# Kernel optimization log

Measured on AMD Instinct MI355X. Metric: run time of the kernel, lower is better.

Reference implementation:

```python
import jax, jax.numpy as jnp
import numpy as np

N, E = 20000, 320000
ATOM_IN, BOND_IN, HIDDEN, LAYERS = 64, 16, 256, 5
BN_EPS = 1e-5


def setup_inputs() -> dict:
    key = jax.random.key(0)
    ks = jax.random.split(key, 16)
    s = 0.05
    return {
        "x": jax.random.normal(ks[0], (N, ATOM_IN), jnp.float32),
        "edge_attr": jax.random.normal(ks[1], (E, BOND_IN), jnp.float32),
        "edge_index": jax.random.randint(ks[2], (2, E), 0, N, jnp.int32),
        "Wa": jax.random.normal(ks[3], (ATOM_IN, HIDDEN), jnp.float32) * s,
        "ba": jnp.zeros((HIDDEN,), jnp.float32),
        "We": jax.random.normal(ks[4], (BOND_IN, HIDDEN), jnp.float32) * s,
        "be": jnp.zeros((HIDDEN,), jnp.float32),
        "eps": jnp.zeros((LAYERS,), jnp.float32),  # train_eps=True, init 0
        "W1": jax.random.normal(ks[5], (LAYERS, HIDDEN, HIDDEN), jnp.float32) * s,
        "b1": jnp.zeros((LAYERS, HIDDEN), jnp.float32),
        "W2": jax.random.normal(ks[6], (LAYERS, HIDDEN, HIDDEN), jnp.float32) * s,
        "b2": jnp.zeros((LAYERS, HIDDEN), jnp.float32),
        "gamma": jnp.ones((LAYERS, HIDDEN), jnp.float32),
        "beta": jnp.zeros((LAYERS, HIDDEN), jnp.float32),
    }


def reference(x, edge_attr, edge_index, Wa, ba, We, be, eps, W1, b1, W2, b2, gamma, beta):
    src, dst = edge_index[0], edge_index[1]  # messages flow src -> dst (PyG x_j = x[src])
    h = x @ Wa + ba                          # [N, H] atom_proj
    e = edge_attr @ We + be                  # [E, H] edge_proj
    for l in range(LAYERS):
        # GINEConv: aggr = sum_j relu(x_j + e_ij); out = mlp((1+eps)*x_i + aggr)
        msg = jax.nn.relu(h[src] + e)                              # [E, H]
        aggr = jax.ops.segment_sum(msg, dst, num_segments=N)        # [N, H]
        z = (1.0 + eps[l]) * h + aggr
        z = jax.nn.relu(z @ W1[l] + b1[l]) @ W2[l] + b2[l]          # 2-layer MLP
        # BatchNorm1d over the node dimension (batch statistics)
        mu = jnp.mean(z, axis=0)
        var = jnp.var(z, axis=0)
        z = (z - mu) * jax.lax.rsqrt(var + BN_EPS) * gamma[l] + beta[l]
        z = jax.nn.relu(z)
        # dropout is identity in deterministic reference (eval)
        h = h + z  # residual
    return h
```

## Files before the change

kernel.cpp:

```cpp
#include <hip/hip_runtime.h>

typedef unsigned short u16;
typedef __attribute__((ext_vector_type(4))) float f32x4;
typedef __attribute__((ext_vector_type(8))) short s16x8;
typedef __attribute__((ext_vector_type(8))) unsigned short u16x8;
typedef __attribute__((ext_vector_type(4))) unsigned short u16x4;

__device__ inline float bf2f(u16 u) {
    unsigned v = ((unsigned)u) << 16;
    return __builtin_bit_cast(float, v);
}
__device__ inline u16 f2bf(float f) {
    unsigned u = __builtin_bit_cast(unsigned, f);
    unsigned r = (u + 0x7FFFu + ((u >> 16) & 1u)) >> 16;
    return (u16)r;
}

__global__ void count_kernel(const int* __restrict__ dst, int E, int* __restrict__ counts) {
    int e = blockIdx.x * 256 + threadIdx.x;
    if (e < E) atomicAdd(&counts[dst[e]], 1);
}

__global__ __launch_bounds__(1024) void scan_kernel(const int* __restrict__ counts,
    int* __restrict__ row_start, int* __restrict__ cursor, int NN) {
    __shared__ int sh[1024];
    const int tid = threadIdx.x;
    const int CH = (NN + 1023) / 1024;
    const int base = tid * CH;
    int sum = 0;
    for (int i = 0; i < CH; ++i) { int idx = base + i; if (idx < NN) sum += counts[idx]; }
    sh[tid] = sum; __syncthreads();
    for (int off = 1; off < 1024; off <<= 1) {
        int v = (tid >= off) ? sh[tid - off] : 0;
        __syncthreads();
        sh[tid] += v;
        __syncthreads();
    }
    int run = sh[tid] - sum;
    for (int i = 0; i < CH; ++i) {
        int idx = base + i;
        if (idx <= NN) {
            row_start[idx] = run;
            if (idx < NN) { cursor[idx] = run; run += counts[idx]; }
        }
    }
}

__global__ void pos_kernel(const int* __restrict__ src, const int* __restrict__ dst, int E,
    int* __restrict__ cursor, int* __restrict__ pos, int* __restrict__ src_perm) {
    int e = blockIdx.x * 256 + threadIdx.x;
    if (e < E) {
        int p = atomicAdd(&cursor[dst[e]], 1);
        pos[e] = p;
        src_perm[p] = src[e];
    }
}

__global__ void prep_kernel(const float* __restrict__ x, const float* __restrict__ Wa,
    const float* __restrict__ We, const float* __restrict__ be,
    const float* __restrict__ W1, const float* __restrict__ W2,
    u16* __restrict__ x_bf, u16* __restrict__ Wat, u16* __restrict__ Wet,
    u16* __restrict__ W1t, u16* __restrict__ W2t, int NN) {
    int i = blockIdx.x * 256 + threadIdx.x;
    const int S0 = NN * 16;
    if (i < S0) {
        f32x4 v = *(const f32x4*)(x + (size_t)i * 4);
        u16x4 o; o.x = f2bf(v[0]); o.y = f2bf(v[1]); o.z = f2bf(v[2]); o.w = f2bf(v[3]);
        *(u16x4*)(x_bf + (size_t)i * 4) = o;
        return;
    }
    i -= S0;
    if (i < 16384) { int n = i >> 6, k = i & 63; Wat[i] = f2bf(Wa[k * 256 + n]); return; }
    i -= 16384;
    if (i < 8192) {
        int n = i >> 5, k = i & 31;
        float v = (k < 16) ? We[k * 256 + n] : ((k == 16) ? be[n] : 0.f);
        Wet[i] = f2bf(v); return;
    }
    i -= 8192;
    if (i < 327680) { int l = i >> 16, r = i & 65535, n = r >> 8, k = r & 255;
        W1t[i] = f2bf(W1[(size_t)l * 65536 + k * 256 + n]); return; }
    i -= 327680;
    if (i < 327680) { int l = i >> 16, r = i & 65535, n = r >> 8, k = r & 255;
        W2t[i] = f2bf(W2[(size_t)l * 65536 + k * 256 + n]); return; }
}

__global__ void permute_pad_eattr_kernel(const float* __restrict__ ea, const int* __restrict__ pos,
                                         int E, u16* __restrict__ out) {
    int e = blockIdx.x * 256 + threadIdx.x;
    if (e >= E) return;
    const float* r = ea + (size_t)e * 16;
    f32x4 q0 = *(const f32x4*)(r + 0);
    f32x4 q1 = *(const f32x4*)(r + 4);
    f32x4 q2 = *(const f32x4*)(r + 8);
    f32x4 q3 = *(const f32x4*)(r + 12);
    u16x8 v0, v1, m, z;
#pragma unroll
    for (int j = 0; j < 4; ++j) {
        v0[j] = f2bf(q0[j]); v0[4 + j] = f2bf(q1[j]);
        v1[j] = f2bf(q2[j]); v1[4 + j] = f2bf(q3[j]);
        m[j] = 0; m[4 + j] = 0; z[j] = 0; z[4 + j] = 0;
    }
    m[0] = 0x3F80;
    u16* o = out + (size_t)pos[e] * 32;
    *(u16x8*)(o + 0) = v0;
    *(u16x8*)(o + 8) = v1;
    *(u16x8*)(o + 16) = m;
    *(u16x8*)(o + 24) = z;
}

__global__ __launch_bounds__(256) void gemm_h0_kernel(
    const u16* __restrict__ A, int lda, int M,
    const u16* __restrict__ Bt, int K,
    const float* __restrict__ bias,
    float* __restrict__ outF, u16* __restrict__ outB, int ldo) {
    __shared__ u16 As[128 * 32];
    __shared__ u16 Bs[128 * 32];
    const int tid = threadIdx.x, lane = tid & 63, wave = tid >> 6;
    const int m0 = blockIdx.x * 128, n0 = blockIdx.y * 128;
    const int wr = (wave >> 1) * 64, wc = (wave & 1) * 64;

    const f32x4 zero4 = {0.f, 0.f, 0.f, 0.f};
    f32x4 acc[4][4];
#pragma unroll
    for (int m = 0; m < 4; ++m)
#pragma unroll
        for (int n = 0; n < 4; ++n) acc[m][n] = zero4;

    for (int k0 = 0; k0 < K; k0 += 32) {
#pragma unroll
        for (int i = 0; i < 2; ++i) {
            int seg = i * 256 + tid;
            int row = seg >> 2, sk = seg & 3;
            int gr = m0 + row; gr = gr < M ? gr : M - 1;
            u16x8 va = *(const u16x8*)(A + (size_t)gr * lda + k0 + sk * 8);
            *(u16x8*)(&As[row * 32 + sk * 8]) = va;
            u16x8 vb = *(const u16x8*)(Bt + (size_t)(n0 + row) * K + k0 + sk * 8);
            *(u16x8*)(&Bs[row * 32 + sk * 8]) = vb;
        }
        __syncthreads();
        const int rsel = lane & 15, koff = (lane >> 4) * 8;
        s16x8 af[4], bf[4];
#pragma unroll
        for (int m = 0; m < 4; ++m) af[m] = *(const s16x8*)(&As[(wr + m * 16 + rsel) * 32 + koff]);
#pragma unroll
        for (int n = 0; n < 4; ++n) bf[n] = *(const s16x8*)(&Bs[(wc + n * 16 + rsel) * 32 + koff]);
#pragma unroll
        for (int m = 0; m < 4; ++m)
#pragma unroll
            for (int n = 0; n < 4; ++n)
                acc[m][n] = __builtin_amdgcn_mfma_f32_16x16x32_bf16(af[m], bf[n], acc[m][n], 0, 0, 0);
        __syncthreads();
    }

    const int cl = lane & 15, rq = lane >> 4;
#pragma unroll
    for (int n = 0; n < 4; ++n) {
        const int gcol = n0 + wc + n * 16 + cl;
        const float bv = bias[gcol];
#pragma unroll
        for (int m = 0; m < 4; ++m) {
#pragma unroll
            for (int j = 0; j < 4; ++j) {
                int grow = m0 + wr + m * 16 + rq * 4 + j;
                if (grow < M) {
                    float v = acc[m][n][j] + bv;
                    outF[(size_t)grow * ldo + gcol] = v;
                    outB[(size_t)grow * ldo + gcol] = f2bf(v);
                }
            }
        }
    }
}

__global__ __launch_bounds__(256) void mlp_fused_kernel(
    const u16* __restrict__ z, int M,
    const u16* __restrict__ W1t, const float* __restrict__ b1,
    const u16* __restrict__ W2t, const float* __restrict__ b2,
    u16* __restrict__ y2,
    float* __restrict__ colsum, float* __restrict__ colsumsq) {
    __shared__ u16 As[64 * 32];
    __shared__ u16 Bs[256 * 32];
    __shared__ u16 Ys[64 * 260];
    const int tid = threadIdx.x, lane = tid & 63, wave = tid >> 6;
    const int m0 = blockIdx.x * 64;
    const int wc = wave * 64;
    const int rsel = lane & 15, koff = (lane >> 4) * 8;
    const int cl = lane & 15, rq = lane >> 4;

    const f32x4 zero4 = {0.f, 0.f, 0.f, 0.f};
    f32x4 acc[4][4];
#pragma unroll
    for (int m = 0; m < 4; ++m)
#pragma unroll
        for (int n = 0; n < 4; ++n) acc[m][n] = zero4;

    for (int k0 = 0; k0 < 256; k0 += 32) {
        {
            int row = tid >> 2, sk = tid & 3;
            int gr = m0 + row; gr = gr < M ? gr : M - 1;
            u16x8 va = *(const u16x8*)(z + (size_t)gr * 256 + k0 + sk * 8);
            *(u16x8*)(&As[row * 32 + sk * 8]) = va;
        }
#pragma unroll
        for (int i = 0; i < 4; ++i) {
            int seg = i * 256 + tid;
            int row = seg >> 2, sk = seg & 3;
            u16x8 vb = *(const u16x8*)(W1t + (size_t)row * 256 + k0 + sk * 8);
            *(u16x8*)(&Bs[row * 32 + sk * 8]) = vb;
        }
        __syncthreads();
        s16x8 af[4], bf[4];
#pragma unroll
        for (int m = 0; m < 4; ++m) af[m] = *(const s16x8*)(&As[(m * 16 + rsel) * 32 + koff]);
#pragma unroll
        for (int n = 0; n < 4; ++n) bf[n] = *(const s16x8*)(&Bs[(wc + n * 16 + rsel) * 32 + koff]);
#pragma unroll
        for (int m = 0; m < 4; ++m)
#pragma unroll
            for (int n = 0; n < 4; ++n)
                acc[m][n] = __builtin_amdgcn_mfma_f32_16x16x32_bf16(af[m], bf[n], acc[m][n], 0, 0, 0);
        __syncthreads();
    }
#pragma unroll
    for (int n = 0; n < 4; ++n) {
        const int gcol = wc + n * 16 + cl;
        const float bv = b1[gcol];
#pragma unroll
        for (int m = 0; m < 4; ++m) {
#pragma unroll
            for (int j = 0; j < 4; ++j) {
                int row = m * 16 + rq * 4 + j;
                float v = fmaxf(acc[m][n][j] + bv, 0.f);
                Ys[row * 260 + gcol] = f2bf(v);
            }
        }
        acc[0][n] = zero4; acc[1][n] = zero4; acc[2][n] = zero4; acc[3][n] = zero4;
    }

    for (int k0 = 0; k0 < 256; k0 += 32) {
#pragma unroll
        for (int i = 0; i < 4; ++i) {
            int seg = i * 256 + tid;
            int row = seg >> 2, sk = seg & 3;
            u16x8 vb = *(const u16x8*)(W2t + (size_t)row * 256 + k0 + sk * 8);
            *(u16x8*)(&Bs[row * 32 + sk * 8]) = vb;
        }
        __syncthreads();
        s16x8 af[4], bf[4];
#pragma unroll
        for (int m = 0; m < 4; ++m) af[m] = *(const s16x8*)(&Ys[(m * 16 + rsel) * 260 + k0 + koff]);
#pragma unroll
        for (int n = 0; n < 4; ++n) bf[n] = *(const s16x8*)(&Bs[(wc + n * 16 + rsel) * 32 + koff]);
#pragma unroll
        for (int m = 0; m < 4; ++m)
#pragma unroll
            for (int n = 0; n < 4; ++n)
                acc[m][n] = __builtin_amdgcn_mfma_f32_16x16x32_bf16(af[m], bf[n], acc[m][n], 0, 0, 0);
        __syncthreads();
    }
#pragma unroll
    for (int n = 0; n < 4; ++n) {
        const int gcol = wc + n * 16 + cl;
        const float bv = b2[gcol];
        float s = 0.f, ss = 0.f;
#pragma unroll
        for (int m = 0; m < 4; ++m) {
#pragma unroll
            for (int j = 0; j < 4; ++j) {
                int row = m * 16 + rq * 4 + j;
                float v = acc[m][n][j] + bv;
                Ys[row * 260 + gcol] = f2bf(v);
                if (m0 + row < M) { s += v; ss += v * v; }
            }
        }
        s += __shfl_down(s, 32); ss += __shfl_down(ss, 32);
        s += __shfl_down(s, 16); ss += __shfl_down(ss, 16);
        if (rq == 0) {
            atomicAdd(&colsum[gcol], s);
            atomicAdd(&colsumsq[gcol], ss);
        }
    }
    __syncthreads();
    for (int r0 = 0; r0 < 64; r0 += 8) {
        int row = r0 + (tid >> 5);
        int gr = m0 + row;
        int cc = (tid & 31) * 8;
        if (gr < M) *(u16x8*)(y2 + (size_t)gr * 256 + cc) = *(u16x8*)(&Ys[row * 260 + cc]);
    }
}

__global__ __launch_bounds__(256) void agg_rc_kernel(
    const int* __restrict__ row_start, const int* __restrict__ src_perm,
    const u16* __restrict__ eap, const u16* __restrict__ Wet,
    const u16* __restrict__ h_bf, const float* __restrict__ h,
    const float* __restrict__ eps, int layer,
    u16* __restrict__ z_bf, int NN) {
    __shared__ u16 ET[4 * 16 * 264];
    const int tid = threadIdx.x;
    const int lane = tid & 63;
    const int wv = tid >> 6;
    const int rsel = lane & 15;
    const int q = lane >> 4;
    const int half = lane >> 5;
    const int c0 = (lane & 31) * 8;
    u16* et = &ET[wv * 16 * 264];

    s16x8 wf[16];
#pragma unroll
    for (int b = 0; b < 16; ++b)
        wf[b] = *(const s16x8*)(Wet + (b * 16 + rsel) * 32 + q * 8);

    const int node = blockIdx.x * 4 + wv;
    if (node >= NN) return;
    const int s0 = row_start[node], s1 = row_start[node + 1];

    const f32x4 zero4 = {0.f, 0.f, 0.f, 0.f};
    float a[8] = {0.f, 0.f, 0.f, 0.f, 0.f, 0.f, 0.f, 0.f};

    for (int e0 = s0; e0 < s1; e0 += 16) {
        const int ec = (e0 + rsel < s1) ? (e0 + rsel) : (s1 - 1);
        s16x8 eaf = *(const s16x8*)(eap + (size_t)ec * 32 + q * 8);
#pragma unroll
        for (int b = 0; b < 16; ++b) {
            f32x4 d = __builtin_amdgcn_mfma_f32_16x16x32_bf16(wf[b], eaf, zero4, 0, 0, 0);
            u16x4 w;
#pragma unroll
            for (int j = 0; j < 4; ++j) w[j] = f2bf(d[j]);
            *(u16x4*)(et + rsel * 264 + b * 16 + q * 4) = w;
        }
        const int cnt = (s1 - e0 < 16) ? (s1 - e0) : 16;
        for (int kk = 0; kk < cnt; kk += 4) {
            const int ka = kk + half, kb = kk + 2 + half;
            const bool v0 = ka < cnt, v1 = kb < cnt;
            const int ia = v0 ? (e0 + ka) : (s1 - 1);
            const int ib = v1 ? (e0 + kb) : (s1 - 1);
            const int sa = src_perm[ia];
            const int sb = src_perm[ib];
            u16x8 h0 = *(const u16x8*)(h_bf + (size_t)sa * 256 + c0);
            u16x8 h1 = *(const u16x8*)(h_bf + (size_t)sb * 256 + c0);
            u16x8 e8a = *(const u16x8*)(et + (v0 ? ka : 0) * 264 + c0);
            u16x8 e8b = *(const u16x8*)(et + (v1 ? kb : 0) * 264 + c0);
            const float m0 = v0 ? 1.f : 0.f;
            const float m1 = v1 ? 1.f : 0.f;
#pragma unroll
            for (int j = 0; j < 8; ++j) {
                a[j] += m0 * fmaxf(bf2f((u16)e8a[j]) + bf2f((u16)h0[j]), 0.f);
                a[j] += m1 * fmaxf(bf2f((u16)e8b[j]) + bf2f((u16)h1[j]), 0.f);
            }
        }
    }
#pragma unroll
    for (int j = 0; j < 8; ++j) a[j] += __shfl_xor(a[j], 32);
    if (half == 0) {
        const float c = 1.f + eps[layer];
        const f32x4 hr0 = *(const f32x4*)(h + (size_t)node * 256 + c0);
        const f32x4 hr1 = *(const f32x4*)(h + (size_t)node * 256 + c0 + 4);
        u16x8 z;
#pragma unroll
        for (int j = 0; j < 4; ++j) {
            z[j] = f2bf(c * hr0[j] + a[j]);
            z[4 + j] = f2bf(c * hr1[j] + a[4 + j]);
        }
        *(u16x8*)(z_bf + (size_t)node * 256 + c0) = z;
    }
}

__global__ __launch_bounds__(256) void bn_res_kernel(
    const u16* __restrict__ y2, const float* __restrict__ colsum,
    const float* __restrict__ colsumsq, const float* __restrict__ gamma,
    const float* __restrict__ beta, const float* __restrict__ hin,
    float* __restrict__ hout, u16* __restrict__ h_bf, int write_bf,
    float invN, int total4) {
    const int i = blockIdx.x * 256 + threadIdx.x;
    if (i >= total4) return;
    const size_t base = (size_t)i * 4;
    const int c0 = (int)(base & 255);
    u16x4 yv = *(const u16x4*)(y2 + base);
    f32x4 hv = *(const f32x4*)(hin + base);
    u16 ys[4] = {yv.x, yv.y, yv.z, yv.w};
    f32x4 res;
#pragma unroll
    for (int j = 0; j < 4; ++j) {
        const int c = c0 + j;
        const float mu = colsum[c] * invN;
        const float var = colsumsq[c] * invN - mu * mu;
        const float sc = gamma[c] * rsqrtf(var + 1e-5f);
        const float sh = beta[c] - mu * sc;
        float v = bf2f(ys[j]) * sc + sh;
        v = fmaxf(v, 0.f);
        res[j] = hv[j] + v;
    }
    *(f32x4*)(hout + base) = res;
    if (write_bf) {
        u16x4 hb; hb.x = f2bf(res[0]); hb.y = f2bf(res[1]); hb.z = f2bf(res[2]); hb.w = f2bf(res[3]);
        *(u16x4*)(h_bf + base) = hb;
    }
}

extern "C" void kernel_launch(void* const* d_in, const int* in_sizes, int n_in,
                              void* d_out, int out_size, void* d_ws, size_t ws_size,
                              hipStream_t stream) {
    const float* x    = (const float*)d_in[0];
    const float* ea   = (const float*)d_in[1];
    const int*   ei   = (const int*)d_in[2];
    const float* Wa   = (const float*)d_in[3];
    const float* ba   = (const float*)d_in[4];
    const float* We   = (const float*)d_in[5];
    const float* be   = (const float*)d_in[6];
    const float* eps  = (const float*)d_in[7];
    const float* W1   = (const float*)d_in[8];
    const float* b1   = (const float*)d_in[9];
    const float* W2   = (const float*)d_in[10];
    const float* b2   = (const float*)d_in[11];
    const float* gamma= (const float*)d_in[12];
    const float* beta = (const float*)d_in[13];

    const int NN = in_sizes[0] / 64;
    const int EE = in_sizes[1] / 16;
    const int* src = ei;
    const int* dst = ei + EE;

    char* p = (char*)d_ws;
    auto alloc = [&](size_t bytes) -> char* {
        char* r = p;
        p += (bytes + 255) & ~(size_t)255;
        return r;
    };
    int*   counts   = (int*)alloc((size_t)(NN + 1) * 4);
    float* colsum   = (float*)alloc(5 * 256 * 4);
    float* colsumsq = (float*)alloc(5 * 256 * 4);
    size_t zbytes   = (size_t)(p - (char*)counts);
    int*   row_start= (int*)alloc((size_t)(NN + 1) * 4);
    int*   cursor   = (int*)alloc((size_t)NN * 4);
    int*   pos      = (int*)alloc((size_t)EE * 4);
    int*   src_perm = (int*)alloc((size_t)EE * 4);
    u16*   x_bf     = (u16*)alloc((size_t)NN * 64 * 2);
    u16*   Wat      = (u16*)alloc(256 * 64 * 2);
    u16*   Wet      = (u16*)alloc(256 * 32 * 2);
    u16*   W1t      = (u16*)alloc((size_t)5 * 65536 * 2);
    u16*   W2t      = (u16*)alloc((size_t)5 * 65536 * 2);
    u16*   eap_perm = (u16*)alloc((size_t)EE * 32 * 2);
    float* h        = (float*)alloc((size_t)NN * 256 * 4);
    u16*   h_bf     = (u16*)alloc((size_t)NN * 256 * 2);
    u16*   z_bf     = (u16*)alloc((size_t)NN * 256 * 2);
    u16*   y2       = (u16*)alloc((size_t)NN * 256 * 2);

    hipMemsetAsync(counts, 0, zbytes, stream);

    const int eb = (EE + 255) / 256;
    count_kernel<<<eb, 256, 0, stream>>>(dst, EE, counts);
    scan_kernel<<<1, 1024, 0, stream>>>(counts, row_start, cursor, NN);
    pos_kernel<<<eb, 256, 0, stream>>>(src, dst, EE, cursor, pos, src_perm);

    const int prep_total = NN * 16 + 16384 + 8192 + 327680 + 327680;
    prep_kernel<<<(prep_total + 255) / 256, 256, 0, stream>>>(
        x, Wa, We, be, W1, W2, x_bf, Wat, Wet, W1t, W2t, NN);
    permute_pad_eattr_kernel<<<eb, 256, 0, stream>>>(ea, pos, EE, eap_perm);

    dim3 gh((NN + 127) / 128, 2);
    gemm_h0_kernel<<<gh, 256, 0, stream>>>(
        x_bf, 64, NN, Wat, 64, ba, h, h_bf, 256);

    const float invN = 1.f / (float)NN;
    const int nb4 = (NN * 64 + 255) / 256;
    const int mlp_blocks = (NN + 63) / 64;
    for (int l = 0; l < 5; ++l) {
        agg_rc_kernel<<<(NN + 3) / 4, 256, 0, stream>>>(
            row_start, src_perm, eap_perm, Wet, h_bf, h, eps, l, z_bf, NN);
        mlp_fused_kernel<<<mlp_blocks, 256, 0, stream>>>(
            z_bf, NN, W1t + (size_t)l * 65536, b1 + l * 256,
            W2t + (size_t)l * 65536, b2 + l * 256, y2,
            colsum + l * 256, colsumsq + l * 256);
        bn_res_kernel<<<nb4, 256, 0, stream>>>(
            y2, colsum + l * 256, colsumsq + l * 256, gamma + l * 256, beta + l * 256,
            h, (l == 4) ? (float*)d_out : h, h_bf, (l < 4) ? 1 : 0, invN, NN * 64);
    }
}
```

Before: 604.0 us.

## Fuse setup kernels, tile weight transpose, read bf16 self term, widen BN vectors

Merges the edge-attribute permute/pad and input/weight preparation into one launch, and replaces the strided per-element W1/W2 transpose with a 32x32 shared-memory tiled transpose. The aggregation kernel now takes the self term from the bf16 copy of h instead of the fp32 copy, which halves that read at the cost of a bit of precision. The BN/residual kernel processes 8 elements per thread with wider vector loads and stores. Together these aim to cut launch overhead and memory traffic in setup and in each layer.

Result: no change. 598.2 us (-1.0%).

```diff
diff --git a/kernel.cpp b/kernel.cpp
--- a/kernel.cpp
+++ b/kernel.cpp
@@ -56,57 +56,71 @@
     }
 }
 
-__global__ void prep_kernel(const float* __restrict__ x, const float* __restrict__ Wa,
-    const float* __restrict__ We, const float* __restrict__ be,
+__global__ __launch_bounds__(256) void setup_fused_kernel(
+    const float* __restrict__ ea, const int* __restrict__ pos, int E, int eb,
+    const float* __restrict__ x, const float* __restrict__ Wa,
+    const float* __restrict__ We, const float* __restrict__ be, int NN, int prepb,
     const float* __restrict__ W1, const float* __restrict__ W2,
-    u16* __restrict__ x_bf, u16* __restrict__ Wat, u16* __restrict__ Wet,
-    u16* __restrict__ W1t, u16* __restrict__ W2t, int NN) {
-    int i = blockIdx.x * 256 + threadIdx.x;
-    const int S0 = NN * 16;
-    if (i < S0) {
-        f32x4 v = *(const f32x4*)(x + (size_t)i * 4);
-        u16x4 o; o.x = f2bf(v[0]); o.y = f2bf(v[1]); o.z = f2bf(v[2]); o.w = f2bf(v[3]);
-        *(u16x4*)(x_bf + (size_t)i * 4) = o;
+    u16* __restrict__ eap_out, u16* __restrict__ x_bf, u16* __restrict__ Wat,
+    u16* __restrict__ Wet, u16* __restrict__ W1t, u16* __restrict__ W2t) {
+    __shared__ float T[32][33];
+    const int b = blockIdx.x;
+    if (b < eb) {
+        int e = b * 256 + threadIdx.x;
+        if (e >= E) return;
+        const float* r = ea + (size_t)e * 16;
+        f32x4 q0 = *(const f32x4*)(r + 0);
+        f32x4 q1 = *(const f32x4*)(r + 4);
+        f32x4 q2 = *(const f32x4*)(r + 8);
+        f32x4 q3 = *(const f32x4*)(r + 12);
+        u16x8 v0, v1, m, z;
+#pragma unroll
+        for (int j = 0; j < 4; ++j) {
+            v0[j] = f2bf(q0[j]); v0[4 + j] = f2bf(q1[j]);
+            v1[j] = f2bf(q2[j]); v1[4 + j] = f2bf(q3[j]);
+            m[j] = 0; m[4 + j] = 0; z[j] = 0; z[4 + j] = 0;
+        }
+        m[0] = 0x3F80;
+        u16* o = eap_out + (size_t)pos[e] * 32;
+        *(u16x8*)(o + 0) = v0;
+        *(u16x8*)(o + 8) = v1;
+        *(u16x8*)(o + 16) = m;
+        *(u16x8*)(o + 24) = z;
         return;
     }
-    i -= S0;
-    if (i < 16384) { int n = i >> 6, k = i & 63; Wat[i] = f2bf(Wa[k * 256 + n]); return; }
-    i -= 16384;
-    if (i < 8192) {
-        int n = i >> 5, k = i & 31;
-        float v = (k < 16) ? We[k * 256 + n] : ((k == 16) ? be[n] : 0.f);
-        Wet[i] = f2bf(v); return;
-    }
-    i -= 8192;
-    if (i < 327680) { int l = i >> 16, r = i & 65535, n = r >> 8, k = r & 255;
-        W1t[i] = f2bf(W1[(size_t)l * 65536 + k * 256 + n]); return; }
-    i -= 327680;
-    if (i < 327680) { int l = i >> 16, r = i & 65535, n = r >> 8, k = r & 255;
-        W2t[i] = f2bf(W2[(size_t)l * 65536 + k * 256 + n]); return; }
-}
-
-__global__ void permute_pad_eattr_kernel(const float* __restrict__ ea, const int* __restrict__ pos,
-                                         int E, u16* __restrict__ out) {
-    int e = blockIdx.x * 256 + threadIdx.x;
-    if (e >= E) return;
-    const float* r = ea + (size_t)e * 16;
-    f32x4 q0 = *(const f32x4*)(r + 0);
-    f32x4 q1 = *(const f32x4*)(r + 4);
-    f32x4 q2 = *(const f32x4*)(r + 8);
-    f32x4 q3 = *(const f32x4*)(r + 12);
-    u16x8 v0, v1, m, z;
-#pragma unroll
-    for (int j = 0; j < 4; ++j) {
-        v0[j] = f2bf(q0[j]); v0[4 + j] = f2bf(q1[j]);
-        v1[j] = f2bf(q2[j]); v1[4 + j] = f2bf(q3[j]);
-        m[j] = 0; m[4 + j] = 0; z[j] = 0; z[4 + j] = 0;
-    }
-    m[0] = 0x3F80;
-    u16* o = out + (size_t)pos[e] * 32;
-    *(u16x8*)(o + 0) = v0;
-    *(u16x8*)(o + 8) = v1;
-    *(u16x8*)(o + 16) = m;
-    *(u16x8*)(o + 24) = z;
+    if (b < eb + prepb) {
+        int i = (b - eb) * 256 + threadIdx.x;
+        const int S0 = NN * 16;
+        if (i < S0) {
+            f32x4 v = *(const f32x4*)(x + (size_t)i * 4);
+            u16x4 o; o.x = f2bf(v[0]); o.y = f2bf(v[1]); o.z = f2bf(v[2]); o.w = f2bf(v[3]);
+            *(u16x4*)(x_bf + (size_t)i * 4) = o;
+            return;
+        }
+        i -= S0;
+        if (i < 16384) { int n = i >> 6, k = i & 63; Wat[i] = f2bf(Wa[k * 256 + n]); return; }
+        i -= 16384;
+        if (i < 8192) {
+            int n = i >> 5, k = i & 31;
+            float v = (k < 16) ? We[k * 256 + n] : ((k == 16) ? be[n] : 0.f);
+            Wet[i] = f2bf(v);
+        }
+        return;
+    }
+    const int bb = b - eb - prepb;
+    const int m5 = bb >> 6;
+    const int rem = bb & 63;
+    const int k0 = (rem & 7) * 32, n0 = (rem >> 3) * 32;
+    const float* srcw = (m5 < 5) ? (W1 + (size_t)m5 * 65536) : (W2 + (size_t)(m5 - 5) * 65536);
+    u16* dstw = (m5 < 5) ? (W1t + (size_t)m5 * 65536) : (W2t + (size_t)(m5 - 5) * 65536);
+    const int tx = threadIdx.x & 31, ty = threadIdx.x >> 5;
+#pragma unroll
+    for (int i = 0; i < 4; ++i)
+        T[ty + 8 * i][tx] = srcw[(size_t)(k0 + ty + 8 * i) * 256 + n0 + tx];
+    __syncthreads();
+#pragma unroll
+    for (int i = 0; i < 4; ++i)
+        dstw[(size_t)(n0 + ty + 8 * i) * 256 + k0 + tx] = f2bf(T[tx][ty + 8 * i]);
 }
 
 __global__ __launch_bounds__(256) void gemm_h0_kernel(
@@ -293,7 +307,7 @@
 __global__ __launch_bounds__(256) void agg_rc_kernel(
     const int* __restrict__ row_start, const int* __restrict__ src_perm,
     const u16* __restrict__ eap, const u16* __restrict__ Wet,
-    const u16* __restrict__ h_bf, const float* __restrict__ h,
+    const u16* __restrict__ h_bf,
     const float* __restrict__ eps, int layer,
     u16* __restrict__ z_bf, int NN) {
     __shared__ u16 ET[4 * 16 * 264];
@@ -354,14 +368,11 @@
     for (int j = 0; j < 8; ++j) a[j] += __shfl_xor(a[j], 32);
     if (half == 0) {
         const float c = 1.f + eps[layer];
-        const f32x4 hr0 = *(const f32x4*)(h + (size_t)node * 256 + c0);
-        const f32x4 hr1 = *(const f32x4*)(h + (size_t)node * 256 + c0 + 4);
+        u16x8 hbv = *(const u16x8*)(h_bf + (size_t)node * 256 + c0);
         u16x8 z;
 #pragma unroll
-        for (int j = 0; j < 4; ++j) {
-            z[j] = f2bf(c * hr0[j] + a[j]);
-            z[4 + j] = f2bf(c * hr1[j] + a[4 + j]);
-        }
+        for (int j = 0; j < 8; ++j)
+            z[j] = f2bf(c * bf2f((u16)hbv[j]) + a[j]);
         *(u16x8*)(z_bf + (size_t)node * 256 + c0) = z;
     }
 }
@@ -371,30 +382,36 @@
     const float* __restrict__ colsumsq, const float* __restrict__ gamma,
     const float* __restrict__ beta, const float* __restrict__ hin,
     float* __restrict__ hout, u16* __restrict__ h_bf, int write_bf,
-    float invN, int total4) {
+    float invN, int total8) {
     const int i = blockIdx.x * 256 + threadIdx.x;
-    if (i >= total4) return;
-    const size_t base = (size_t)i * 4;
+    if (i >= total8) return;
+    const size_t base = (size_t)i * 8;
     const int c0 = (int)(base & 255);
-    u16x4 yv = *(const u16x4*)(y2 + base);
-    f32x4 hv = *(const f32x4*)(hin + base);
-    u16 ys[4] = {yv.x, yv.y, yv.z, yv.w};
-    f32x4 res;
-#pragma unroll
-    for (int j = 0; j < 4; ++j) {
+    u16x8 yv = *(const u16x8*)(y2 + base);
+    f32x4 hv0 = *(const f32x4*)(hin + base);
+    f32x4 hv1 = *(const f32x4*)(hin + base + 4);
+    float res[8];
+#pragma unroll
+    for (int j = 0; j < 8; ++j) {
         const int c = c0 + j;
         const float mu = colsum[c] * invN;
         const float var = colsumsq[c] * invN - mu * mu;
         const float sc = gamma[c] * rsqrtf(var + 1e-5f);
         const float sh = beta[c] - mu * sc;
-        float v = bf2f(ys[j]) * sc + sh;
+        float v = bf2f((u16)yv[j]) * sc + sh;
         v = fmaxf(v, 0.f);
-        res[j] = hv[j] + v;
-    }
-    *(f32x4*)(hout + base) = res;
+        res[j] = ((j < 4) ? hv0[j] : hv1[j - 4]) + v;
+    }
+    f32x4 o0, o1;
+#pragma unroll
+    for (int j = 0; j < 4; ++j) { o0[j] = res[j]; o1[j] = res[4 + j]; }
+    *(f32x4*)(hout + base) = o0;
+    *(f32x4*)(hout + base + 4) = o1;
     if (write_bf) {
-        u16x4 hb; hb.x = f2bf(res[0]); hb.y = f2bf(res[1]); hb.z = f2bf(res[2]); hb.w = f2bf(res[3]);
-        *(u16x4*)(h_bf + base) = hb;
+        u16x8 hb;
+#pragma unroll
+        for (int j = 0; j < 8; ++j) hb[j] = f2bf(res[j]);
+        *(u16x8*)(h_bf + base) = hb;
     }
 }
 
@@ -453,27 +470,29 @@
     scan_kernel<<<1, 1024, 0, stream>>>(counts, row_start, cursor, NN);
     pos_kernel<<<eb, 256, 0, stream>>>(src, dst, EE, cursor, pos, src_perm);
 
-    const int prep_total = NN * 16 + 16384 + 8192 + 327680 + 327680;
-    prep_kernel<<<(prep_total + 255) / 256, 256, 0, stream>>>(
-        x, Wa, We, be, W1, W2, x_bf, Wat, Wet, W1t, W2t, NN);
-    permute_pad_eattr_kernel<<<eb, 256, 0, stream>>>(ea, pos, EE, eap_perm);
+    const int prep_total = NN * 16 + 16384 + 8192;
+    const int prepb = (prep_total + 255) / 256;
+    const int setup_blocks = eb + prepb + 640;
+    setup_fused_kernel<<<setup_blocks, 256, 0, stream>>>(
+        ea, pos, EE, eb, x, Wa, We, be, NN, prepb, W1, W2,
+        eap_perm, x_bf, Wat, Wet, W1t, W2t);
 
     dim3 gh((NN + 127) / 128, 2);
     gemm_h0_kernel<<<gh, 256, 0, stream>>>(
         x_bf, 64, NN, Wat, 64, ba, h, h_bf, 256);
 
     const float invN = 1.f / (float)NN;
-    const int nb4 = (NN * 64 + 255) / 256;
+    const int nb8 = (NN * 32 + 255) / 256;
     const int mlp_blocks = (NN + 63) / 64;
     for (int l = 0; l < 5; ++l) {
         agg_rc_kernel<<<(NN + 3) / 4, 256, 0, stream>>>(
-            row_start, src_perm, eap_perm, Wet, h_bf, h, eps, l, z_bf, NN);
+            row_start, src_perm, eap_perm, Wet, h_bf, eps, l, z_bf, NN);
         mlp_fused_kernel<<<mlp_blocks, 256, 0, stream>>>(
             z_bf, NN, W1t + (size_t)l * 65536, b1 + l * 256,
             W2t + (size_t)l * 65536, b2 + l * 256, y2,
             colsum + l * 256, colsumsq + l * 256);
-        bn_res_kernel<<<nb4, 256, 0, stream>>>(
+        bn_res_kernel<<<nb8, 256, 0, stream>>>(
             y2, colsum + l * 256, colsumsq + l * 256, gamma + l * 256, beta + l * 256,
-            h, (l == 4) ? (float*)d_out : h, h_bf, (l < 4) ? 1 : 0, invN, NN * 64);
-    }
-}
+            h, (l == 4) ? (float*)d_out : h, h_bf, (l < 4) ? 1 : 0, invN, NN * 32);
+    }
+}
```
